# Kernel tuning notes

Hardware: AMD Instinct MI355X
Metric: run time of the kernel (lower is better)

The kernel has to match this reference:

```python
import jax, jax.numpy as jnp
import numpy as np

B, N, D, R, W, H, I = 256, 2048, 128, 4, 1, 1024, 1024
CI = I + R * D                       # controller input size (1536)
IF = 2 * D * W + 2 * W + 1 + 4 * R + D * R   # interface size (787)
OPI = H + R * D                      # output_proj input (1536)


def _norm(v):
    # F.normalize(dim=-1): x / max(||x||, eps)
    return v / jnp.maximum(jnp.linalg.norm(v, axis=-1, keepdims=True), 1e-12)


def setup_inputs() -> dict:
    key = jax.random.key(0)
    ks = jax.random.split(key, 16)
    u = lambda k, shape, fan: jax.random.uniform(k, shape, jnp.float32, -1.0 / np.sqrt(fan), 1.0 / np.sqrt(fan))
    return {
        "x": jax.random.normal(ks[0], (B, I), jnp.float32),
        "memory": jax.random.normal(ks[1], (N, D), jnp.float32) * np.sqrt(2.0 / (N + D)),  # xavier-ish
        "usage": jax.random.uniform(ks[2], (N,), jnp.float32),          # usage in [0,1)
        "link": jax.random.normal(ks[3], (N, N), jnp.float32) * 0.01,   # non-trivial link state
        "W_ih": u(ks[4], (4 * H, CI), H),
        "W_hh": u(ks[5], (4 * H, H), H),
        "b_ih": u(ks[6], (4 * H,), H),
        "b_hh": u(ks[7], (4 * H,), H),
        "W_if": u(ks[8], (IF, H), H),
        "b_if": u(ks[9], (IF,), H),
        "W_out": u(ks[10], (H, OPI), OPI),
        "b_out": u(ks[11], (H,), OPI),
    }


def reference(x, memory, usage, link, W_ih, W_hh, b_ih, b_hh, W_if, b_if, W_out, b_out):
    # initial uniform read weights (prev state at first step)
    prev_rw = jnp.full((B, R, N), 1.0 / N, x.dtype)
    read_flat = (prev_rw @ memory).reshape(B, -1)                 # (B, R*D)
    cin = jnp.concatenate([x, read_flat], axis=-1)                # (B, CI)

    # single LSTM step, h0 = c0 = 0, torch gate order i,f,g,o
    g = cin @ W_ih.T + b_ih + b_hh
    gi, gf, gg, go = jnp.split(g, 4, axis=-1)
    c = jax.nn.sigmoid(gi) * jnp.tanh(gg)
    h = jax.nn.sigmoid(go) * jnp.tanh(c)                          # (B, H) controller out

    itf = h @ W_if.T + b_if                                       # (B, IF)
    o = 0
    write_vals = itf[:, o:o + D * W].reshape(B, W, D); o += D * W
    erase = jax.nn.sigmoid(itf[:, o:o + D * W]).reshape(B, W, D); o += D * W
    write_gates = jax.nn.sigmoid(itf[:, o:o + W]); o += W         # (B, W)
    alloc_gate = jax.nn.sigmoid(itf[:, o:o + 1]); o += 1          # (B, 1)
    o += W                                                        # free gates (parsed, unused)
    read_modes = jax.nn.softmax(itf[:, o:o + 3 * R].reshape(B, R, 3), -1); o += 3 * R
    read_str = jax.nn.softplus(itf[:, o:o + R]); o += R           # (B, R)
    read_keys = itf[:, o:o + D * R].reshape(B, R, D)

    # content addressing for the write (strength = 1)
    mem_n = _norm(memory)
    cw = jax.nn.softmax(_norm(write_vals.mean(1)) @ mem_n.T, -1)  # (B, N)

    # allocation weighting: sorted-usage cumprod (per source semantics)
    idx = jnp.argsort(usage)
    su = usage[idx]
    cp = jnp.cumprod(1.0 - su)
    alloc_s = jnp.concatenate([su[:1], su[1:] * cp[:-1]])
    alloc = jnp.zeros_like(usage).at[idx].set(alloc_s)[None, :] * alloc_gate  # (B, N)

    write_w = write_gates[:, :, None] * (0.5 * cw + 0.5 * alloc)[:, None, :]  # (B, W, N)

    # temporal link update: batch-mean of diag-masked outer product, decay 0.9
    lu = jnp.einsum('bwn,bwm->nm', write_w, write_w) / B
    lu = lu * (1.0 - jnp.eye(N, dtype=lu.dtype))
    link_new = link * 0.9 + lu * 0.1

    # memory write (erase then add, batch-mean)
    ev = erase * write_gates[:, :, None]
    av = write_vals * write_gates[:, :, None]
    erase_mat = jnp.einsum('bwn,bwd->nd', write_w, ev) / B
    add_mat = jnp.einsum('bwn,bwd->nd', write_w, av) / B
    mem_new = memory * (1.0 - erase_mat) + add_mat

    # read addressing on updated memory and updated link (all R heads vectorized)
    sim = jnp.einsum('brd,nd->brn', _norm(read_keys), _norm(mem_new))
    content_r = jax.nn.softmax(sim * read_str[:, :, None], -1)    # (B, R, N)
    backward_w = jnp.einsum('brn,nm->brm', prev_rw, link_new)     # mode 1: prev @ L
    forward_w = jnp.einsum('brn,mn->brm', prev_rw, link_new)      # mode 2: prev @ L^T
    new_rw = (read_modes[..., 0:1] * content_r
              + read_modes[..., 1:2] * backward_w
              + read_modes[..., 2:3] * forward_w)                 # (B, R, N)

    read_out = (new_rw @ mem_new).reshape(B, -1)                  # (B, R*D)
    out = jnp.concatenate([h, read_out], axis=-1) @ W_out.T + b_out
    return out
```

## Files before the change

### kernel.cpp

```cpp
#include <hip/hip_runtime.h>
#include <cmath>

#define DEVI __device__ __forceinline__

DEVI float sigm(float x){ return 1.f/(1.f+expf(-x)); }

typedef __attribute__((ext_vector_type(8))) _Float16 half8;
typedef __attribute__((ext_vector_type(4))) _Float16 half4;
typedef __attribute__((ext_vector_type(4))) float float4v;


__global__ void k_zero(float* __restrict__ p, int n){
  int i = blockIdx.x*256 + threadIdx.x;
  if (i < n) p[i] = 0.f;
}

__global__ __launch_bounds__(256) void k_stage1(
    const float* __restrict__ mem, float* __restrict__ cm, _Float16* __restrict__ mem_h,
    const float* __restrict__ usage, float* __restrict__ alloc,
    const float* __restrict__ link, float* __restrict__ rsl, float* __restrict__ cslp)
{
  __shared__ float smem[4][132];
  const int blk = blockIdx.x, t = threadIdx.x;
  const int wv = t >> 6, lane = t & 63;

  if (blk < 128){
    int rbase = blk*16 + wv*4;
    float x0[4], x1[4], ss[4];
    #pragma unroll
    for (int u = 0; u < 4; u++){
      const float* a = mem + (size_t)(rbase+u)*128;
      x0[u] = a[lane]; x1[u] = a[lane+64];
    }
    #pragma unroll
    for (int u = 0; u < 4; u++) ss[u] = x0[u]*x0[u] + x1[u]*x1[u];
    #pragma unroll
    for (int o = 1; o < 64; o <<= 1){
      #pragma unroll
      for (int u = 0; u < 4; u++) ss[u] += __shfl_xor(ss[u], o);
    }
    float c0 = 0.f, c1 = 0.f;
    #pragma unroll
    for (int u = 0; u < 4; u++){
      float invn = 1.f / fmaxf(sqrtf(ss[u]), 1e-12f);
      mem_h[(size_t)(rbase+u)*128 + lane]      = (_Float16)(x0[u]*invn);
      mem_h[(size_t)(rbase+u)*128 + 64 + lane] = (_Float16)(x1[u]*invn);
      c0 += x0[u]; c1 += x1[u];
    }
    smem[wv][lane] = c0; smem[wv][64+lane] = c1;
    __syncthreads();
    if (t < 128) atomicAdd(&cm[t], smem[0][t]+smem[1][t]+smem[2][t]+smem[3][t]);
  } else if (blk < 384){
    int pb = blk - 128;
    int r0 = pb*8;
    int c0 = t*8;
    float4v v0[8], v1[8];
    #pragma unroll
    for (int u = 0; u < 8; u++){
      const float* lp = link + (size_t)(r0+u)*2048 + c0;
      v0[u] = *(const float4v*)lp;
      v1[u] = *(const float4v*)(lp+4);
    }
    float colacc[8];
    #pragma unroll
    for (int j = 0; j < 8; j++) colacc[j] = 0.f;
    float rowpart[8];
    #pragma unroll
    for (int u = 0; u < 8; u++){
      float s = 0.f;
      #pragma unroll
      for (int j = 0; j < 4; j++){
        colacc[j]   += v0[u][j]; colacc[4+j] += v1[u][j];
        s += v0[u][j] + v1[u][j];
      }
      rowpart[u] = s;
    }
    #pragma unroll
    for (int o = 1; o < 64; o <<= 1){
      #pragma unroll
      for (int u = 0; u < 8; u++) rowpart[u] += __shfl_xor(rowpart[u], o);
    }
    if (lane == 0){
      #pragma unroll
      for (int u = 0; u < 8; u++) smem[wv][u] = rowpart[u];
    }
    __syncthreads();
    if (t < 8) rsl[r0+t] = smem[0][t]+smem[1][t]+smem[2][t]+smem[3][t];
    float4v w0, w1;
    #pragma unroll
    for (int j = 0; j < 4; j++){ w0[j] = colacc[j]; w1[j] = colacc[4+j]; }
    *(float4v*)&cslp[(size_t)pb*2048 + c0]     = w0;
    *(float4v*)&cslp[(size_t)pb*2048 + c0 + 4] = w1;
  } else {
    int n = (blk - 384)*4 + wv;
    float un = usage[n];
    float prod = 1.f;
    #pragma unroll
    for (int i = 0; i < 32; i++){
      int m = lane + i*64;
      float um = usage[m];
      bool before = (um < un) || (um == un && m < n);
      prod *= before ? (1.f - um) : 1.f;
    }
    #pragma unroll
    for (int o = 32; o > 0; o >>= 1) prod *= __shfl_xor(prod, o);
    if (lane == 0) alloc[n] = un * prod;
  }
}

#define QA 264
#define QB 520
#define QB3 776

template<typename TB> struct BReg;
template<> struct BReg<_Float16>{
  half8 v;
  DEVI void load(const _Float16* p){ v = *(const half8*)p; }
  DEVI half8 get() const { return v; }
};
template<> struct BReg<float>{
  float4v a, b;
  DEVI void load(const float* p){ a = *(const float4v*)p; b = *(const float4v*)(p+4); }
  DEVI half8 get() const {
    half8 h;
    #pragma unroll
    for (int j = 0; j < 4; j++){ h[j] = (_Float16)a[j]; h[4+j] = (_Float16)b[j]; }
    return h;
  }
};

struct ARegX {
  float4v a, b; float sc;
  DEVI void load(const float* __restrict__ x, const float* __restrict__ cm, int row, int k){
    const float* p;
    if (k < 1024){ p = x + (size_t)row*1024 + k; sc = 1.f; }
    else         { p = cm + ((k - 1024) & 127); sc = (1.f/2048.f); }
    a = *(const float4v*)p; b = *(const float4v*)(p+4);
  }
  DEVI half8 get() const {
    half8 h;
    #pragma unroll
    for (int j = 0; j < 4; j++){ h[j] = (_Float16)(a[j]*sc); h[4+j] = (_Float16)(b[j]*sc); }
    return h;
  }
};

template<typename TB>
__global__ __launch_bounds__(256) void gemm_t(
    const _Float16* __restrict__ A, const TB* __restrict__ Bm, float* __restrict__ C,
    int M, int N, int K,
    const float* __restrict__ bias1, const float* __restrict__ bias2)
{
  __shared__ _Float16 Ah[2][8*QA];
  __shared__ _Float16 Bh[2][8*QB];
  const int tid = threadIdx.x;
  const int m0 = blockIdx.y*32, n0 = blockIdx.x*64;
  const int T = K >> 6;
  const int arow = tid >> 3, aq = tid & 7;
  const int brow = tid >> 3, bq = tid & 7;
  int nB0 = n0 + brow;      if (nB0 >= N) nB0 = N - 1;
  int nB1 = n0 + brow + 32; if (nB1 >= N) nB1 = N - 1;
  const _Float16* Aptr = A + (size_t)(m0 + arow)*K + aq*8;
  const TB* Bp0 = Bm + (size_t)nB0*K + bq*8;
  const TB* Bp1 = Bm + (size_t)nB1*K + bq*8;
  const int wA  = aq*QA + arow*8;
  const int wB0 = bq*QB + brow*8;
  const int wB1 = bq*QB + (brow+32)*8;
  const int wv_ = tid >> 6, lane = tid & 63;
  const int fq = lane >> 4, fr = lane & 15;
  const int m16 = (wv_ & 1)*16, nb = (wv_ >> 1)*32;

  half8 ra;
  BReg<TB> rb0, rb1;
  ra = *(const half8*)(Aptr);
  rb0.load(Bp0);
  rb1.load(Bp1);
  *(half8*)&Ah[0][wA]  = ra;
  *(half8*)&Bh[0][wB0] = rb0.get();
  *(half8*)&Bh[0][wB1] = rb1.get();
  __syncthreads();

  float4v acc0 = {0.f,0.f,0.f,0.f}, acc1 = {0.f,0.f,0.f,0.f};
  for (int t = 0; t < T; t++){
    const int cur = t & 1, nxt = cur ^ 1;
    if (t+1 < T){
      ra = *(const half8*)(Aptr + (t+1)*64);
      rb0.load(Bp0 + (t+1)*64);
      rb1.load(Bp1 + (t+1)*64);
    }
    #pragma unroll
    for (int s = 0; s < 2; s++){
      int q = s*4 + fq;
      half8 a  = *(half8*)&Ah[cur][q*QA + (m16+fr)*8];
      half8 b0 = *(half8*)&Bh[cur][q*QB + (nb+fr)*8];
      half8 b1 = *(half8*)&Bh[cur][q*QB + (nb+16+fr)*8];
      acc0 = __builtin_amdgcn_mfma_f32_16x16x32_f16(a, b0, acc0, 0, 0, 0);
      acc1 = __builtin_amdgcn_mfma_f32_16x16x32_f16(a, b1, acc1, 0, 0, 0);
    }
    if (t+1 < T){
      *(half8*)&Ah[nxt][wA]  = ra;
      *(half8*)&Bh[nxt][wB0] = rb0.get();
      *(half8*)&Bh[nxt][wB1] = rb1.get();
    }
    __syncthreads();
  }

  const int colA = n0 + nb + fr, colB = colA + 16;
  #pragma unroll
  for (int i = 0; i < 4; i++){
    int m = m0 + m16 + fq*4 + i;
    if (colA < N){
      float v = acc0[i];
      if (bias1) v += bias1[colA];
      if (bias2) v += bias2[colA];
      C[(size_t)m*N + colA] = v;
    }
    if (colB < N){
      float v = acc1[i];
      if (bias1) v += bias1[colB];
      if (bias2) v += bias2[colB];
      C[(size_t)m*N + colB] = v;
    }
  }
}

__global__ __launch_bounds__(256) void k_gemm_wwExp(
    const _Float16* __restrict__ A, const _Float16* __restrict__ Bm,
    float* __restrict__ C, float* __restrict__ rsum)
{
  __shared__ _Float16 Ah[2][8*QA];
  __shared__ _Float16 Bh[2][8*QB];
  const int tid = threadIdx.x;
  const int m0 = blockIdx.y*32, n0 = blockIdx.x*64;
  const int arow = tid >> 3, aq = tid & 7;
  const int brow = tid >> 3, bq = tid & 7;
  const _Float16* Aptr = A + (size_t)(m0 + arow)*128 + aq*8;
  const _Float16* Bp0 = Bm + (size_t)(n0 + brow)*128 + bq*8;
  const _Float16* Bp1 = Bm + (size_t)(n0 + brow + 32)*128 + bq*8;
  const int wA  = aq*QA + arow*8;
  const int wB0 = bq*QB + brow*8;
  const int wB1 = bq*QB + (brow+32)*8;
  const int wv_ = tid >> 6, lane = tid & 63;
  const int fq = lane >> 4, fr = lane & 15;
  const int m16 = (wv_ & 1)*16, nb = (wv_ >> 1)*32;

  half8 ra  = *(const half8*)(Aptr);
  half8 rb0 = *(const half8*)(Bp0);
  half8 rb1 = *(const half8*)(Bp1);
  *(half8*)&Ah[0][wA]  = ra;
  *(half8*)&Bh[0][wB0] = rb0;
  *(half8*)&Bh[0][wB1] = rb1;
  __syncthreads();

  float4v acc0 = {0.f,0.f,0.f,0.f}, acc1 = {0.f,0.f,0.f,0.f};
  for (int t = 0; t < 2; t++){
    const int cur = t & 1, nxt = cur ^ 1;
    if (t == 0){
      ra  = *(const half8*)(Aptr + 64);
      rb0 = *(const half8*)(Bp0 + 64);
      rb1 = *(const half8*)(Bp1 + 64);
    }
    #pragma unroll
    for (int s = 0; s < 2; s++){
      int q = s*4 + fq;
      half8 a  = *(half8*)&Ah[cur][q*QA + (m16+fr)*8];
      half8 b0 = *(half8*)&Bh[cur][q*QB + (nb+fr)*8];
      half8 b1 = *(half8*)&Bh[cur][q*QB + (nb+16+fr)*8];
      acc0 = __builtin_amdgcn_mfma_f32_16x16x32_f16(a, b0, acc0, 0, 0, 0);
      acc1 = __builtin_amdgcn_mfma_f32_16x16x32_f16(a, b1, acc1, 0, 0, 0);
    }
    if (t == 0){
      *(half8*)&Ah[nxt][wA]  = ra;
      *(half8*)&Bh[nxt][wB0] = rb0;
      *(half8*)&Bh[nxt][wB1] = rb1;
    }
    __syncthreads();
  }

  const int colA = n0 + nb + fr, colB = colA + 16;
  #pragma unroll
  for (int i = 0; i < 4; i++){
    int m = m0 + m16 + fq*4 + i;
    float e0 = expf(acc0[i]);
    float e1 = expf(acc1[i]);
    C[(size_t)m*2048 + colA] = e0;
    C[(size_t)m*2048 + colB] = e1;
    float rs = e0 + e1;
    #pragma unroll
    for (int o = 1; o < 16; o <<= 1) rs += __shfl_xor(rs, o);
    if (fr == 0) atomicAdd(&rsum[m], rs);
  }
}

__global__ __launch_bounds__(256) void k_gemm_lstm(
    const float* __restrict__ x, const float* __restrict__ cm,
    const float* __restrict__ W,
    const float* __restrict__ b_ih, const float* __restrict__ b_hh,
    _Float16* __restrict__ h)
{
  __shared__ _Float16 Ah[2][8*QA];
  __shared__ _Float16 Bh[2][8*QB3];
  const int tid = threadIdx.x;
  const int m0 = blockIdx.y*32, c0 = blockIdx.x*32;
  const int T = 24;
  const int arow = tid >> 3, aq = tid & 7;
  const int brow = tid >> 3, bq = tid & 7;
  const int arw = m0 + arow;
  const float* Bpi = W + (size_t)(       c0 + brow)*1536 + bq*8;
  const float* Bpg = W + (size_t)(2048 + c0 + brow)*1536 + bq*8;
  const float* Bpo = W + (size_t)(3072 + c0 + brow)*1536 + bq*8;
  const int wA  = aq*QA + arow*8;
  const int wBi = bq*QB3 + brow*8;
  const int wBg = bq*QB3 + (32+brow)*8;
  const int wBo = bq*QB3 + (64+brow)*8;
  const int wv_ = tid >> 6, lane = tid & 63;
  const int fq = lane >> 4, fr = lane & 15;
  const int m16 = (wv_ & 1)*16, c16 = (wv_ >> 1)*16;

  ARegX ax0, ax1;
  BReg<float> ri0, rg0, ro0, ri1, rg1, ro1;
  ax0.load(x, cm, arw, aq*8);
  ri0.load(Bpi); rg0.load(Bpg); ro0.load(Bpo);
  ax1.load(x, cm, arw, aq*8 + 64);
  ri1.load(Bpi + 64); rg1.load(Bpg + 64); ro1.load(Bpo + 64);
  *(half8*)&Ah[0][wA]  = ax0.get();
  *(half8*)&Bh[0][wBi] = ri0.get();
  *(half8*)&Bh[0][wBg] = rg0.get();
  *(half8*)&Bh[0][wBo] = ro0.get();
  __syncthreads();

  float4v acci = {0.f,0.f,0.f,0.f}, accg = {0.f,0.f,0.f,0.f}, acco = {0.f,0.f,0.f,0.f};
  for (int t = 0; t < T; t++){
    const int cur = t & 1, nxt = cur ^ 1;
    if (t+2 < T){
      if (cur == 0){
        ax0.load(x, cm, arw, aq*8 + (t+2)*64);
        ri0.load(Bpi + (t+2)*64); rg0.load(Bpg + (t+2)*64); ro0.load(Bpo + (t+2)*64);
      } else {
        ax1.load(x, cm, arw, aq*8 + (t+2)*64);
        ri1.load(Bpi + (t+2)*64); rg1.load(Bpg + (t+2)*64); ro1.load(Bpo + (t+2)*64);
      }
    }
    #pragma unroll
    for (int s = 0; s < 2; s++){
      int q = s*4 + fq;
      half8 a  = *(half8*)&Ah[cur][q*QA + (m16+fr)*8];
      half8 bi = *(half8*)&Bh[cur][q*QB3 + (c16+fr)*8];
      half8 bg = *(half8*)&Bh[cur][q*QB3 + (32+c16+fr)*8];
      half8 bo = *(half8*)&Bh[cur][q*QB3 + (64+c16+fr)*8];
      acci = __builtin_amdgcn_mfma_f32_16x16x32_f16(a, bi, acci, 0, 0, 0);
      accg = __builtin_amdgcn_mfma_f32_16x16x32_f16(a, bg, accg, 0, 0, 0);
      acco = __builtin_amdgcn_mfma_f32_16x16x32_f16(a, bo, acco, 0, 0, 0);
    }
    if (t+1 < T){
      if (nxt == 1){
        *(half8*)&Ah[1][wA]  = ax1.get();
        *(half8*)&Bh[1][wBi] = ri1.get();
        *(half8*)&Bh[1][wBg] = rg1.get();
        *(half8*)&Bh[1][wBo] = ro1.get();
      } else {
        *(half8*)&Ah[0][wA]  = ax0.get();
        *(half8*)&Bh[0][wBi] = ri0.get();
        *(half8*)&Bh[0][wBg] = rg0.get();
        *(half8*)&Bh[0][wBo] = ro0.get();
      }
    }
    __syncthreads();
  }

  const int col = c0 + c16 + fr;
  const float bi1 = b_ih[col]        + b_hh[col];
  const float bg1 = b_ih[2048 + col] + b_hh[2048 + col];
  const float bo1 = b_ih[3072 + col] + b_hh[3072 + col];
  #pragma unroll
  for (int i = 0; i < 4; i++){
    int m = m0 + m16 + fq*4 + i;
    float gi = acci[i] + bi1;
    float gg = accg[i] + bg1;
    float go = acco[i] + bo1;
    float c = sigm(gi) * tanhf(gg);
    h[(size_t)m*1024 + col] = (_Float16)(sigm(go) * tanhf(c));
  }
}

DEVI float blockReduce128(float v, float* lds2){
  #pragma unroll
  for (int o = 32; o > 0; o >>= 1) v += __shfl_xor(v, o);
  int w = threadIdx.x >> 6;
  __syncthreads();
  if ((threadIdx.x & 63) == 0) lds2[w] = v;
  __syncthreads();
  return lds2[0] + lds2[1];
}

__global__ __launch_bounds__(128) void k_parse(const float* __restrict__ itf,
    _Float16* __restrict__ wv_h, float* __restrict__ ev, float* __restrict__ av,
    float* __restrict__ wg_, float* __restrict__ ag_,
    float* __restrict__ rm0, float* __restrict__ rm1, float* __restrict__ rm2,
    _Float16* __restrict__ rks_h)
{
  __shared__ float red[2];
  int b = blockIdx.x, t = threadIdx.x;
  const float* it = itf + (size_t)b*787;
  float wg = sigm(it[256]);
  float ag = sigm(it[257]);
  if (t == 0){ wg_[b] = wg; ag_[b] = ag; }
  float w = it[t];
  av[b*128 + t] = w * wg;
  ev[b*128 + t] = sigm(it[128 + t]) * wg;
  float ss = blockReduce128(w*w, red);
  float invwv = 1.f / fmaxf(sqrtf(ss), 1e-12f);
  wv_h[b*128 + t] = (_Float16)(w * invwv);
  if (t < 4){
    int rr = t;
    float m0v = it[259 + rr*3 + 0], m1v = it[259 + rr*3 + 1], m2v = it[259 + rr*3 + 2];
    float mx = fmaxf(m0v, fmaxf(m1v, m2v));
    float e0 = expf(m0v - mx), e1 = expf(m1v - mx), e2 = expf(m2v - mx);
    float inv = 1.f / (e0 + e1 + e2);
    rm0[b*4 + rr] = e0*inv; rm1[b*4 + rr] = e1*inv; rm2[b*4 + rr] = e2*inv;
  }
  #pragma unroll
  for (int rr = 0; rr < 4; rr++){
    float kv = it[275 + rr*128 + t];
    float ks = blockReduce128(kv*kv, red);
    float sx = it[271 + rr];
    float str = fmaxf(sx, 0.f) + log1pf(expf(-fabsf(sx)));
    float invk = 1.f / fmaxf(sqrtf(ks), 1e-12f);
    rks_h[((size_t)b*4 + rr)*128 + t] = (_Float16)(kv * invk * str);
  }
}

__global__ __launch_bounds__(256) void k_memupdate_fused(const float* __restrict__ ww,
    const float* __restrict__ ev, const float* __restrict__ av,
    const float* __restrict__ mem,
    const float* __restrict__ wg, const float* __restrict__ ag,
    const float* __restrict__ alloc, const float* __restrict__ rsum,
    const float* __restrict__ rsl, const float* __restrict__ cslp,
    _Float16* __restrict__ memn_h, _Float16* __restrict__ memnT_h,
    float* __restrict__ bwm, float* __restrict__ fwm)
{
  __shared__ float Ws[16][34];
  __shared__ float Es[16][132], Vs[16][132];
  __shared__ float lb[128], lf[128];
  __shared__ _Float16 Traw[32][132];
  __shared__ float tbs[256], c1s[256], c2s[256];
  __shared__ float allocL[32];
  __shared__ float sq[8][32], sd[8][32];
  __shared__ float cpart[8][32];
  __shared__ float bwL[32], fwL[32];
  __shared__ float sred[4];
  const int n0 = blockIdx.x*32;
  const int tid = threadIdx.x, tx = tid & 31, ty = tid >> 5;

  {
    float sa = 0.f;
    #pragma unroll
    for (int i = 0; i < 8; i++) sa += alloc[tid + i*256];
    #pragma unroll
    for (int o = 32; o > 0; o >>= 1) sa += __shfl_xor(sa, o);
    if ((tid & 63) == 0) sred[tid >> 6] = sa;
    if (tid < 128){ lb[tid] = 0.f; lf[tid] = 0.f; }
    if (tid < 32) allocL[tid] = alloc[n0 + tid];
    __syncthreads();
    sa = (sred[0]+sred[1]) + (sred[2]+sred[3]);
    float w = wg[tid], a = ag[tid];
    tbs[tid] = w*(0.5f + 0.5f*a*sa);
    c1s[tid] = 0.5f*w / rsum[tid];
    c2s[tid] = 0.5f*w*a;
  }
  {
    int col = n0 + tx;
    float s = 0.f;
    for (int p = ty*32; p < ty*32 + 32; p += 4){
      s += cslp[(size_t)(p+0)*2048 + col] + cslp[(size_t)(p+1)*2048 + col]
         + cslp[(size_t)(p+2)*2048 + col] + cslp[(size_t)(p+3)*2048 + col];
    }
    cpart[ty][tx] = s;
  }
  __syncthreads();

  const int wk = tid >> 4, wn = (tid & 15)*2;
  const int ek = tid >> 4, ec = (tid & 15)*8;
  float ae[4][4] = {}, aa[4][4] = {};
  float qp = 0.f, ddp = 0.f;
  for (int k0 = 0; k0 < 256; k0 += 16){
    float2 vw  = *(const float2*)(ww + (size_t)(k0+wk)*2048 + n0 + wn);
    float4 ve0 = *(const float4*)(ev + (size_t)(k0+ek)*128 + ec);
    float4 ve1 = *(const float4*)(ev + (size_t)(k0+ek)*128 + ec + 4);
    float4 va0 = *(const float4*)(av + (size_t)(k0+ek)*128 + ec);
    float4 va1 = *(const float4*)(av + (size_t)(k0+ek)*128 + ec + 4);
    __syncthreads();
    {
      float cb1 = c1s[k0+wk], cb2 = c2s[k0+wk];
      Ws[wk][wn]   = cb1*vw.x + cb2*allocL[wn];
      Ws[wk][wn+1] = cb1*vw.y + cb2*allocL[wn+1];
    }
    *(float4*)&Es[ek][ec] = ve0; *(float4*)&Es[ek][ec+4] = ve1;
    *(float4*)&Vs[ek][ec] = va0; *(float4*)&Vs[ek][ec+4] = va1;
    __syncthreads();
    #pragma unroll
    for (int k = 0; k < 16; k++){
      float a[4], e[4], v[4];
      #pragma unroll
      for (int i = 0; i < 4; i++) a[i] = Ws[k][ty*4+i];
      #pragma unroll
      for (int j = 0; j < 4; j++){ e[j] = Es[k][tx*4+j]; v[j] = Vs[k][tx*4+j]; }
      #pragma unroll
      for (int i = 0; i < 4; i++)
        #pragma unroll
        for (int j = 0; j < 4; j++){
          ae[i][j] = fmaf(a[i], e[j], ae[i][j]);
          aa[i][j] = fmaf(a[i], v[j], aa[i][j]);
        }
    }
    {
      float w0 = Ws[ty*2+0][tx], w1 = Ws[ty*2+1][tx];
      qp  = fmaf(tbs[k0+ty*2+0], w0, qp);  ddp = fmaf(w0, w0, ddp);
      qp  = fmaf(tbs[k0+ty*2+1], w1, qp);  ddp = fmaf(w1, w1, ddp);
    }
  }
  sq[ty][tx] = qp; sd[ty][tx] = ddp;
  __syncthreads();
  if (tid < 32){
    float q = 0.f, dd = 0.f, cs = 0.f;
    #pragma unroll
    for (int z = 0; z < 8; z++){ q += sq[z][tid]; dd += sd[z][tid]; cs += cpart[z][tid]; }
    float lus = (q - dd) * (1.f/256.f);
    bwL[tid] = (0.9f*cs + 0.1f*lus) * (1.f/2048.f);
    fwL[tid] = (0.9f*rsl[n0+tid] + 0.1f*lus) * (1.f/2048.f);
  }
  __syncthreads();

  float ab[4] = {0,0,0,0}, af[4] = {0,0,0,0};
  #pragma unroll
  for (int i = 0; i < 4; i++){
    int n = n0 + ty*4 + i;
    float bwn = bwL[ty*4+i], fwn = fwL[ty*4+i];
    float v[4]; float ss = 0.f;
    #pragma unroll
    for (int j = 0; j < 4; j++){
      int d = tx*4 + j;
      float em = ae[i][j]*(1.f/256.f), am = aa[i][j]*(1.f/256.f);
      float mv = mem[(size_t)n*128 + d]*(1.f - em) + am;
      v[j] = mv; ss += mv*mv;
      ab[j] = fmaf(bwn, mv, ab[j]);
      af[j] = fmaf(fwn, mv, af[j]);
    }
    #pragma unroll
    for (int o = 1; o < 32; o <<= 1) ss += __shfl_xor(ss, o);
    float invn = 1.f / fmaxf(sqrtf(ss), 1e-12f);
    half4 hn, hr;
    #pragma unroll
    for (int j = 0; j < 4; j++){ hn[j] = (_Float16)(v[j]*invn); hr[j] = (_Float16)v[j]; }
    *(half4*)(memn_h + (size_t)n*128 + tx*4) = hn;
    *(half4*)&Traw[ty*4+i][tx*4] = hr;
  }
  __syncthreads();
  {
    int d = tid >> 1, seg = (tid & 1)*16;
    half8 o0, o1;
    #pragma unroll
    for (int j = 0; j < 8; j++){ o0[j] = Traw[seg+j][d]; o1[j] = Traw[seg+8+j][d]; }
    *(half8*)(memnT_h + (size_t)d*2048 + n0 + seg)     = o0;
    *(half8*)(memnT_h + (size_t)d*2048 + n0 + seg + 8) = o1;
  }
  #pragma unroll
  for (int j = 0; j < 4; j++){
    atomicAdd(&lb[tx*4+j], ab[j]);
    atomicAdd(&lf[tx*4+j], af[j]);
  }
  __syncthreads();
  if (tid < 128){
    atomicAdd(&bwm[tid], lb[tid]);
    atomicAdd(&fwm[tid], lf[tid]);
  }
}

__global__ __launch_bounds__(256) void k_flash(
    const _Float16* __restrict__ Q, const _Float16* __restrict__ Kh,
    const _Float16* __restrict__ Vt,
    float* __restrict__ pacc, float* __restrict__ pm, float* __restrict__ pl)
{
  __shared__ _Float16 Pl[4][16][32];
  __shared__ float cmb[4][2080];
  __shared__ float scl[4][16];
  const int tid = threadIdx.x;
  const int qt = blockIdx.x >> 2, kc = blockIdx.x & 3;
  const int wv = tid >> 6, lane = tid & 63;
  const int fq = lane >> 4, fr = lane & 15;
  const int kw0 = kc*512 + wv*128;

  half8 aq[4];
  #pragma unroll
  for (int c = 0; c < 4; c++)
    aq[c] = *(const half8*)(Q + (size_t)(qt*16 + fr)*128 + c*32 + fq*8);

  float m[4] = {-3.0e38f,-3.0e38f,-3.0e38f,-3.0e38f};
  float l[4] = {0.f,0.f,0.f,0.f};
  float4v acc[8] = {};
  for (int s = 0; s < 4; s++){
    const int kb = kw0 + s*32;
    float4v S0 = {0,0,0,0}, S1 = {0,0,0,0};
    #pragma unroll
    for (int c = 0; c < 4; c++){
      half8 b0 = *(const half8*)(Kh + (size_t)(kb + fr)*128      + c*32 + fq*8);
      half8 b1 = *(const half8*)(Kh + (size_t)(kb + 16 + fr)*128 + c*32 + fq*8);
      S0 = __builtin_amdgcn_mfma_f32_16x16x32_f16(aq[c], b0, S0, 0, 0, 0);
      S1 = __builtin_amdgcn_mfma_f32_16x16x32_f16(aq[c], b1, S1, 0, 0, 0);
    }
    float mt[4], ps[4];
    #pragma unroll
    for (int i = 0; i < 4; i++) mt[i] = fmaxf(S0[i], S1[i]);
    #pragma unroll
    for (int o = 1; o < 16; o <<= 1){
      #pragma unroll
      for (int i = 0; i < 4; i++) mt[i] = fmaxf(mt[i], __shfl_xor(mt[i], o));
    }
    #pragma unroll
    for (int i = 0; i < 4; i++){
      float mn = fmaxf(m[i], mt[i]);
      float al = expf(m[i] - mn);
      float p0 = expf(S0[i] - mn), p1 = expf(S1[i] - mn);
      S0[i] = p0; S1[i] = p1;
      ps[i] = p0 + p1;
      l[i] *= al;
      m[i] = mn;
      #pragma unroll
      for (int c = 0; c < 8; c++) acc[c][i] *= al;
    }
    #pragma unroll
    for (int o = 1; o < 16; o <<= 1){
      #pragma unroll
      for (int i = 0; i < 4; i++) ps[i] += __shfl_xor(ps[i], o);
    }
    #pragma unroll
    for (int i = 0; i < 4; i++) l[i] += ps[i];
    #pragma unroll
    for (int i = 0; i < 4; i++){
      Pl[wv][fq*4+i][fr]      = (_Float16)S0[i];
      Pl[wv][fq*4+i][16 + fr] = (_Float16)S1[i];
    }
    half8 pf = *(half8*)&Pl[wv][fr][fq*8];
    #pragma unroll
    for (int c = 0; c < 8; c++){
      half8 bv = *(const half8*)(Vt + (size_t)(c*16 + fr)*2048 + kb + fq*8);
      acc[c] = __builtin_amdgcn_mfma_f32_16x16x32_f16(pf, bv, acc[c], 0, 0, 0);
    }
  }
  if (fr == 0){
    #pragma unroll
    for (int i = 0; i < 4; i++){
      cmb[wv][fq*4+i]      = m[i];
      cmb[wv][16 + fq*4+i] = l[i];
    }
  }
  #pragma unroll
  for (int c = 0; c < 8; c++)
    #pragma unroll
    for (int i = 0; i < 4; i++)
      cmb[wv][32 + (fq*4+i)*128 + c*16 + fr] = acc[c][i];
  __syncthreads();
  if (tid < 16){
    float mm = fmaxf(fmaxf(cmb[0][tid], cmb[1][tid]), fmaxf(cmb[2][tid], cmb[3][tid]));
    float ll = 0.f;
    #pragma unroll
    for (int w = 0; w < 4; w++){
      float e = expf(cmb[w][tid] - mm);
      scl[w][tid] = e;
      ll += e * cmb[w][16 + tid];
    }
    pm[blockIdx.x*16 + tid] = mm;
    pl[blockIdx.x*16 + tid] = ll;
  }
  __syncthreads();
  for (int e = tid; e < 2048; e += 256){
    int q = e >> 7;
    float a = scl[0][q]*cmb[0][32+e] + scl[1][q]*cmb[1][32+e]
            + scl[2][q]*cmb[2][32+e] + scl[3][q]*cmb[3][32+e];
    pacc[(size_t)blockIdx.x*2048 + e] = a;
  }
}

__global__ void k_hro_comb(const _Float16* __restrict__ h, const float* __restrict__ pacc,
                           const float* __restrict__ pm, const float* __restrict__ pl,
                           const float* __restrict__ rm0, const float* __restrict__ rm1,
                           const float* __restrict__ rm2, const float* __restrict__ bwm,
                           const float* __restrict__ fwm, _Float16* __restrict__ hro){
  int idx = blockIdx.x*256 + threadIdx.x;
  int b = idx / 1536, k = idx - b*1536;
  if (k < 1024){
    hro[idx] = h[b*1024 + k];
  } else {
    int r = k - 1024, rh = r >> 7, d = r & 127;
    int row = b*4 + rh, qt = row >> 4, q = row & 15;
    float mm = -3.0e38f;
    #pragma unroll
    for (int kc = 0; kc < 4; kc++) mm = fmaxf(mm, pm[(qt*4+kc)*16 + q]);
    float num = 0.f, den = 0.f;
    #pragma unroll
    for (int kc = 0; kc < 4; kc++){
      float e = expf(pm[(qt*4+kc)*16 + q] - mm);
      den += e * pl[(qt*4+kc)*16 + q];
      num += e * pacc[(size_t)(qt*4+kc)*2048 + q*128 + d];
    }
    float pv = num / den;
    hro[idx] = (_Float16)(rm0[row]*pv + rm1[row]*bwm[d] + rm2[row]*fwm[d]);
  }
}


extern "C" void kernel_launch(void* const* d_in, const int* in_sizes, int n_in,
                              void* d_out, int out_size, void* d_ws, size_t ws_size,
                              hipStream_t stream)
{
  const float* x     = (const float*)d_in[0];
  const float* mem   = (const float*)d_in[1];
  const float* usage = (const float*)d_in[2];
  const float* link  = (const float*)d_in[3];
  const float* W_ih  = (const float*)d_in[4];
  const float* b_ih  = (const float*)d_in[6];
  const float* b_hh  = (const float*)d_in[7];
  const float* W_if  = (const float*)d_in[8];
  const float* b_if  = (const float*)d_in[9];
  const float* W_out = (const float*)d_in[10];
  const float* b_out = (const float*)d_in[11];
  float* out = (float*)d_out;
  float* ws  = (float*)d_ws;

  float* cm     = ws + 0;
  float* bwm    = ws + 2176;
  float* fwm    = ws + 2304;
  float* rsum   = ws + 2432;
  float* wg     = ws + 6784;
  float* ag     = ws + 7040;
  float* rm0    = ws + 7296;
  float* rm1    = ws + 8320;
  float* rm2    = ws + 9344;
  float* alloc  = ws + 10368;
  float* rsl    = ws + 12416;
  float* ev     = ws + 14464;
  float* av     = ws + 47232;
  float* itf    = ws + 1128576;
  float* ww     = ws + 1330048;
  float* pacc   = ws + 1854336;
  float* pm     = ws + 2378624;
  float* pl     = ws + 2382720;
  _Float16* wv_h    = (_Float16*)(ws + 2386816);
  _Float16* mem_h   = (_Float16*)(ws + 2403200);
  _Float16* memn_h  = (_Float16*)(ws + 2534272);
  _Float16* memnT_h = (_Float16*)(ws + 2665344);
  _Float16* rks_h   = (_Float16*)(ws + 2796416);
  _Float16* hro_h   = (_Float16*)(ws + 2861952);
  _Float16* h_h     = (_Float16*)(ws + 3255168);
  float* cslp       = ws + 3386240;

  k_zero<<<11, 256, 0, stream>>>(ws, 2688);

  k_stage1<<<896, 256, 0, stream>>>(mem, cm, mem_h, usage, alloc, link, rsl, cslp);

  k_gemm_lstm<<<dim3(32,8), 256, 0, stream>>>(x, cm, W_ih, b_ih, b_hh, h_h);

  gemm_t<float><<<dim3(13,8), 256, 0, stream>>>(h_h, W_if, itf, 256, 787, 1024, b_if, nullptr);
  k_parse<<<256, 128, 0, stream>>>(itf, wv_h, ev, av, wg, ag, rm0, rm1, rm2, rks_h);

  k_gemm_wwExp<<<dim3(32,8), 256, 0, stream>>>(wv_h, mem_h, ww, rsum);

  k_memupdate_fused<<<64, 256, 0, stream>>>(ww, ev, av, mem, wg, ag, alloc, rsum,
                                            rsl, cslp, memn_h, memnT_h, bwm, fwm);

  k_flash<<<256, 256, 0, stream>>>(rks_h, memn_h, memnT_h, pacc, pm, pl);

  k_hro_comb<<<1536, 256, 0, stream>>>(h_h, pacc, pm, pl, rm0, rm1, rm2, bwm, fwm, hro_h);
  gemm_t<float><<<dim3(16,8), 256, 0, stream>>>(hro_h, W_out, out, 256, 1024, 1536, b_out, nullptr);

  (void)in_sizes; (void)n_in; (void)out_size; (void)ws_size;
}
```

Before: 233.8 us.

## Co-schedule link/alloc reductions with LSTM GEMM and drop h copy before output GEMM

```diff
diff --git a/kernel.cpp b/kernel.cpp
--- a/kernel.cpp
+++ b/kernel.cpp
@@ -16,96 +16,36 @@
 }
 
 __global__ __launch_bounds__(256) void k_stage1(
-    const float* __restrict__ mem, float* __restrict__ cm, _Float16* __restrict__ mem_h,
-    const float* __restrict__ usage, float* __restrict__ alloc,
-    const float* __restrict__ link, float* __restrict__ rsl, float* __restrict__ cslp)
+    const float* __restrict__ mem, float* __restrict__ cm, _Float16* __restrict__ mem_h)
 {
   __shared__ float smem[4][132];
   const int blk = blockIdx.x, t = threadIdx.x;
   const int wv = t >> 6, lane = t & 63;
-
-  if (blk < 128){
-    int rbase = blk*16 + wv*4;
-    float x0[4], x1[4], ss[4];
-    #pragma unroll
-    for (int u = 0; u < 4; u++){
-      const float* a = mem + (size_t)(rbase+u)*128;
-      x0[u] = a[lane]; x1[u] = a[lane+64];
-    }
-    #pragma unroll
-    for (int u = 0; u < 4; u++) ss[u] = x0[u]*x0[u] + x1[u]*x1[u];
-    #pragma unroll
-    for (int o = 1; o < 64; o <<= 1){
-      #pragma unroll
-      for (int u = 0; u < 4; u++) ss[u] += __shfl_xor(ss[u], o);
-    }
-    float c0 = 0.f, c1 = 0.f;
-    #pragma unroll
-    for (int u = 0; u < 4; u++){
-      float invn = 1.f / fmaxf(sqrtf(ss[u]), 1e-12f);
-      mem_h[(size_t)(rbase+u)*128 + lane]      = (_Float16)(x0[u]*invn);
-      mem_h[(size_t)(rbase+u)*128 + 64 + lane] = (_Float16)(x1[u]*invn);
-      c0 += x0[u]; c1 += x1[u];
-    }
-    smem[wv][lane] = c0; smem[wv][64+lane] = c1;
-    __syncthreads();
-    if (t < 128) atomicAdd(&cm[t], smem[0][t]+smem[1][t]+smem[2][t]+smem[3][t]);
-  } else if (blk < 384){
-    int pb = blk - 128;
-    int r0 = pb*8;
-    int c0 = t*8;
-    float4v v0[8], v1[8];
-    #pragma unroll
-    for (int u = 0; u < 8; u++){
-      const float* lp = link + (size_t)(r0+u)*2048 + c0;
-      v0[u] = *(const float4v*)lp;
-      v1[u] = *(const float4v*)(lp+4);
-    }
-    float colacc[8];
-    #pragma unroll
-    for (int j = 0; j < 8; j++) colacc[j] = 0.f;
-    float rowpart[8];
-    #pragma unroll
-    for (int u = 0; u < 8; u++){
-      float s = 0.f;
-      #pragma unroll
-      for (int j = 0; j < 4; j++){
-        colacc[j]   += v0[u][j]; colacc[4+j] += v1[u][j];
-        s += v0[u][j] + v1[u][j];
-      }
-      rowpart[u] = s;
-    }
-    #pragma unroll
-    for (int o = 1; o < 64; o <<= 1){
-      #pragma unroll
-      for (int u = 0; u < 8; u++) rowpart[u] += __shfl_xor(rowpart[u], o);
-    }
-    if (lane == 0){
-      #pragma unroll
-      for (int u = 0; u < 8; u++) smem[wv][u] = rowpart[u];
-    }
-    __syncthreads();
-    if (t < 8) rsl[r0+t] = smem[0][t]+smem[1][t]+smem[2][t]+smem[3][t];
-    float4v w0, w1;
-    #pragma unroll
-    for (int j = 0; j < 4; j++){ w0[j] = colacc[j]; w1[j] = colacc[4+j]; }
-    *(float4v*)&cslp[(size_t)pb*2048 + c0]     = w0;
-    *(float4v*)&cslp[(size_t)pb*2048 + c0 + 4] = w1;
-  } else {
-    int n = (blk - 384)*4 + wv;
-    float un = usage[n];
-    float prod = 1.f;
-    #pragma unroll
-    for (int i = 0; i < 32; i++){
-      int m = lane + i*64;
-      float um = usage[m];
-      bool before = (um < un) || (um == un && m < n);
-      prod *= before ? (1.f - um) : 1.f;
-    }
-    #pragma unroll
-    for (int o = 32; o > 0; o >>= 1) prod *= __shfl_xor(prod, o);
-    if (lane == 0) alloc[n] = un * prod;
-  }
+  int rbase = blk*16 + wv*4;
+  float x0[4], x1[4], ss[4];
+  #pragma unroll
+  for (int u = 0; u < 4; u++){
+    const float* a = mem + (size_t)(rbase+u)*128;
+    x0[u] = a[lane]; x1[u] = a[lane+64];
+  }
+  #pragma unroll
+  for (int u = 0; u < 4; u++) ss[u] = x0[u]*x0[u] + x1[u]*x1[u];
+  #pragma unroll
+  for (int o = 1; o < 64; o <<= 1){
+    #pragma unroll
+    for (int u = 0; u < 4; u++) ss[u] += __shfl_xor(ss[u], o);
+  }
+  float c0 = 0.f, c1 = 0.f;
+  #pragma unroll
+  for (int u = 0; u < 4; u++){
+    float invn = 1.f / fmaxf(sqrtf(ss[u]), 1e-12f);
+    mem_h[(size_t)(rbase+u)*128 + lane]      = (_Float16)(x0[u]*invn);
+    mem_h[(size_t)(rbase+u)*128 + 64 + lane] = (_Float16)(x1[u]*invn);
+    c0 += x0[u]; c1 += x1[u];
+  }
+  smem[wv][lane] = c0; smem[wv][64+lane] = c1;
+  __syncthreads();
+  if (t < 128) atomicAdd(&cm[t], smem[0][t]+smem[1][t]+smem[2][t]+smem[3][t]);
 }
 
 #define QA 264
@@ -224,6 +164,78 @@
   }
 }
 
+__global__ __launch_bounds__(256) void gemm_hro(
+    const _Float16* __restrict__ Ah_, const _Float16* __restrict__ Aro,
+    const float* __restrict__ Bm, float* __restrict__ C,
+    const float* __restrict__ bias1)
+{
+  __shared__ _Float16 Ah[2][8*QA];
+  __shared__ _Float16 Bh[2][8*QB];
+  const int tid = threadIdx.x;
+  const int m0 = blockIdx.y*32, n0 = blockIdx.x*64;
+  const int T = 24;
+  const int arow = tid >> 3, aq = tid & 7;
+  const int brow = tid >> 3, bq = tid & 7;
+  const int arw = m0 + arow;
+  const float* Bp0 = Bm + (size_t)(n0 + brow)*1536 + bq*8;
+  const float* Bp1 = Bm + (size_t)(n0 + brow + 32)*1536 + bq*8;
+  const int wA  = aq*QA + arow*8;
+  const int wB0 = bq*QB + brow*8;
+  const int wB1 = bq*QB + (brow+32)*8;
+  const int wv_ = tid >> 6, lane = tid & 63;
+  const int fq = lane >> 4, fr = lane & 15;
+  const int m16 = (wv_ & 1)*16, nb = (wv_ >> 1)*32;
+
+  auto ldA = [&](int k) -> half8 {
+    const _Float16* p = (k < 1024) ? (Ah_ + (size_t)arw*1024 + k)
+                                   : (Aro + (size_t)arw*512 + (k - 1024));
+    return *(const half8*)p;
+  };
+
+  half8 ra;
+  BReg<float> rb0, rb1;
+  ra = ldA(aq*8);
+  rb0.load(Bp0);
+  rb1.load(Bp1);
+  *(half8*)&Ah[0][wA]  = ra;
+  *(half8*)&Bh[0][wB0] = rb0.get();
+  *(half8*)&Bh[0][wB1] = rb1.get();
+  __syncthreads();
+
+  float4v acc0 = {0.f,0.f,0.f,0.f}, acc1 = {0.f,0.f,0.f,0.f};
+  for (int t = 0; t < T; t++){
+    const int cur = t & 1, nxt = cur ^ 1;
+    if (t+1 < T){
+      ra = ldA(aq*8 + (t+1)*64);
+      rb0.load(Bp0 + (t+1)*64);
+      rb1.load(Bp1 + (t+1)*64);
+    }
+    #pragma unroll
+    for (int s = 0; s < 2; s++){
+      int q = s*4 + fq;
+      half8 a  = *(half8*)&Ah[cur][q*QA + (m16+fr)*8];
+      half8 b0 = *(half8*)&Bh[cur][q*QB + (nb+fr)*8];
+      half8 b1 = *(half8*)&Bh[cur][q*QB + (nb+16+fr)*8];
+      acc0 = __builtin_amdgcn_mfma_f32_16x16x32_f16(a, b0, acc0, 0, 0, 0);
+      acc1 = __builtin_amdgcn_mfma_f32_16x16x32_f16(a, b1, acc1, 0, 0, 0);
+    }
+    if (t+1 < T){
+      *(half8*)&Ah[nxt][wA]  = ra;
+      *(half8*)&Bh[nxt][wB0] = rb0.get();
+      *(half8*)&Bh[nxt][wB1] = rb1.get();
+    }
+    __syncthreads();
+  }
+
+  const int colA = n0 + nb + fr, colB = colA + 16;
+  #pragma unroll
+  for (int i = 0; i < 4; i++){
+    int m = m0 + m16 + fq*4 + i;
+    C[(size_t)m*1024 + colA] = acc0[i] + bias1[colA];
+    C[(size_t)m*1024 + colB] = acc1[i] + bias1[colB];
+  }
+}
+
 __global__ __launch_bounds__(256) void k_gemm_wwExp(
     const _Float16* __restrict__ A, const _Float16* __restrict__ Bm,
     float* __restrict__ C, float* __restrict__ rsum)
@@ -292,94 +304,157 @@
   }
 }
 
-__global__ __launch_bounds__(256) void k_gemm_lstm(
+__global__ __launch_bounds__(256) void k_big2(
     const float* __restrict__ x, const float* __restrict__ cm,
     const float* __restrict__ W,
     const float* __restrict__ b_ih, const float* __restrict__ b_hh,
-    _Float16* __restrict__ h)
+    _Float16* __restrict__ h,
+    const float* __restrict__ usage, float* __restrict__ alloc,
+    const float* __restrict__ link, float* __restrict__ rsl, float* __restrict__ cslp)
 {
-  __shared__ _Float16 Ah[2][8*QA];
-  __shared__ _Float16 Bh[2][8*QB3];
-  const int tid = threadIdx.x;
-  const int m0 = blockIdx.y*32, c0 = blockIdx.x*32;
-  const int T = 24;
-  const int arow = tid >> 3, aq = tid & 7;
-  const int brow = tid >> 3, bq = tid & 7;
-  const int arw = m0 + arow;
-  const float* Bpi = W + (size_t)(       c0 + brow)*1536 + bq*8;
-  const float* Bpg = W + (size_t)(2048 + c0 + brow)*1536 + bq*8;
-  const float* Bpo = W + (size_t)(3072 + c0 + brow)*1536 + bq*8;
-  const int wA  = aq*QA + arow*8;
-  const int wBi = bq*QB3 + brow*8;
-  const int wBg = bq*QB3 + (32+brow)*8;
-  const int wBo = bq*QB3 + (64+brow)*8;
-  const int wv_ = tid >> 6, lane = tid & 63;
-  const int fq = lane >> 4, fr = lane & 15;
-  const int m16 = (wv_ & 1)*16, c16 = (wv_ >> 1)*16;
-
-  ARegX ax0, ax1;
-  BReg<float> ri0, rg0, ro0, ri1, rg1, ro1;
-  ax0.load(x, cm, arw, aq*8);
-  ri0.load(Bpi); rg0.load(Bpg); ro0.load(Bpo);
-  ax1.load(x, cm, arw, aq*8 + 64);
-  ri1.load(Bpi + 64); rg1.load(Bpg + 64); ro1.load(Bpo + 64);
-  *(half8*)&Ah[0][wA]  = ax0.get();
-  *(half8*)&Bh[0][wBi] = ri0.get();
-  *(half8*)&Bh[0][wBg] = rg0.get();
-  *(half8*)&Bh[0][wBo] = ro0.get();
-  __syncthreads();
-
-  float4v acci = {0.f,0.f,0.f,0.f}, accg = {0.f,0.f,0.f,0.f}, acco = {0.f,0.f,0.f,0.f};
-  for (int t = 0; t < T; t++){
-    const int cur = t & 1, nxt = cur ^ 1;
-    if (t+2 < T){
-      if (cur == 0){
-        ax0.load(x, cm, arw, aq*8 + (t+2)*64);
-        ri0.load(Bpi + (t+2)*64); rg0.load(Bpg + (t+2)*64); ro0.load(Bpo + (t+2)*64);
-      } else {
-        ax1.load(x, cm, arw, aq*8 + (t+2)*64);
-        ri1.load(Bpi + (t+2)*64); rg1.load(Bpg + (t+2)*64); ro1.load(Bpo + (t+2)*64);
+  extern __shared__ char smraw[];
+  const int blk = blockIdx.x, tid = threadIdx.x;
+  const int wv = tid >> 6, lane = tid & 63;
+
+  if (blk < 256){
+    _Float16* AhP = (_Float16*)smraw;
+    _Float16* BhP = (_Float16*)(smraw + 2*8*QA*sizeof(_Float16));
+    const int SA = 8*QA, SB = 8*QB3;
+    const int m0 = (blk >> 5)*32, c0 = (blk & 31)*32;
+    const int T = 24;
+    const int arow = tid >> 3, aq = tid & 7;
+    const int brow = tid >> 3, bq = tid & 7;
+    const int arw = m0 + arow;
+    const float* Bpi = W + (size_t)(       c0 + brow)*1536 + bq*8;
+    const float* Bpg = W + (size_t)(2048 + c0 + brow)*1536 + bq*8;
+    const float* Bpo = W + (size_t)(3072 + c0 + brow)*1536 + bq*8;
+    const int wA  = aq*QA + arow*8;
+    const int wBi = bq*QB3 + brow*8;
+    const int wBg = bq*QB3 + (32+brow)*8;
+    const int wBo = bq*QB3 + (64+brow)*8;
+    const int fq = lane >> 4, fr = lane & 15;
+    const int m16 = (wv & 1)*16, c16 = (wv >> 1)*16;
+
+    ARegX ax0, ax1;
+    BReg<float> ri0, rg0, ro0, ri1, rg1, ro1;
+    ax0.load(x, cm, arw, aq*8);
+    ri0.load(Bpi); rg0.load(Bpg); ro0.load(Bpo);
+    ax1.load(x, cm, arw, aq*8 + 64);
+    ri1.load(Bpi + 64); rg1.load(Bpg + 64); ro1.load(Bpo + 64);
+    *(half8*)&AhP[wA]  = ax0.get();
+    *(half8*)&BhP[wBi] = ri0.get();
+    *(half8*)&BhP[wBg] = rg0.get();
+    *(half8*)&BhP[wBo] = ro0.get();
+    __syncthreads();
+
+    float4v acci = {0.f,0.f,0.f,0.f}, accg = {0.f,0.f,0.f,0.f}, acco = {0.f,0.f,0.f,0.f};
+    for (int t = 0; t < T; t++){
+      const int cur = t & 1, nxt = cur ^ 1;
+      if (t+2 < T){
+        if (cur == 0){
+          ax0.load(x, cm, arw, aq*8 + (t+2)*64);
+          ri0.load(Bpi + (t+2)*64); rg0.load(Bpg + (t+2)*64); ro0.load(Bpo + (t+2)*64);
+        } else {
+          ax1.load(x, cm, arw, aq*8 + (t+2)*64);
+          ri1.load(Bpi + (t+2)*64); rg1.load(Bpg + (t+2)*64); ro1.load(Bpo + (t+2)*64);
+        }
       }
-    }
-    #pragma unroll
-    for (int s = 0; s < 2; s++){
-      int q = s*4 + fq;
-      half8 a  = *(half8*)&Ah[cur][q*QA + (m16+fr)*8];
-      half8 bi = *(half8*)&Bh[cur][q*QB3 + (c16+fr)*8];
-      half8 bg = *(half8*)&Bh[cur][q*QB3 + (32+c16+fr)*8];
-      half8 bo = *(half8*)&Bh[cur][q*QB3 + (64+c16+fr)*8];
-      acci = __builtin_amdgcn_mfma_f32_16x16x32_f16(a, bi, acci, 0, 0, 0);
-      accg = __builtin_amdgcn_mfma_f32_16x16x32_f16(a, bg, accg, 0, 0, 0);
-      acco = __builtin_amdgcn_mfma_f32_16x16x32_f16(a, bo, acco, 0, 0, 0);
-    }
-    if (t+1 < T){
-      if (nxt == 1){
-        *(half8*)&Ah[1][wA]  = ax1.get();
-        *(half8*)&Bh[1][wBi] = ri1.get();
-        *(half8*)&Bh[1][wBg] = rg1.get();
-        *(half8*)&Bh[1][wBo] = ro1.get();
-      } else {
-        *(half8*)&Ah[0][wA]  = ax0.get();
-        *(half8*)&Bh[0][wBi] = ri0.get();
-        *(half8*)&Bh[0][wBg] = rg0.get();
-        *(half8*)&Bh[0][wBo] = ro0.get();
+      #pragma unroll
+      for (int s = 0; s < 2; s++){
+        int q = s*4 + fq;
+        half8 a  = *(half8*)&AhP[cur*SA + q*QA + (m16+fr)*8];
+        half8 bi = *(half8*)&BhP[cur*SB + q*QB3 + (c16+fr)*8];
+        half8 bg = *(half8*)&BhP[cur*SB + q*QB3 + (32+c16+fr)*8];
+        half8 bo = *(half8*)&BhP[cur*SB + q*QB3 + (64+c16+fr)*8];
+        acci = __builtin_amdgcn_mfma_f32_16x16x32_f16(a, bi, acci, 0, 0, 0);
+        accg = __builtin_amdgcn_mfma_f32_16x16x32_f16(a, bg, accg, 0, 0, 0);
+        acco = __builtin_amdgcn_mfma_f32_16x16x32_f16(a, bo, acco, 0, 0, 0);
       }
+      if (t+1 < T){
+        if (nxt == 1){
+          *(half8*)&AhP[SA + wA]  = ax1.get();
+          *(half8*)&BhP[SB + wBi] = ri1.get();
+          *(half8*)&BhP[SB + wBg] = rg1.get();
+          *(half8*)&BhP[SB + wBo] = ro1.get();
+        } else {
+          *(half8*)&AhP[wA]  = ax0.get();
+          *(half8*)&BhP[wBi] = ri0.get();
+          *(half8*)&BhP[wBg] = rg0.get();
+          *(half8*)&BhP[wBo] = ro0.get();
+        }
+      }
+      __syncthreads();
+    }
+
+    const int col = c0 + c16 + fr;
+    const float bi1 = b_ih[col]        + b_hh[col];
+    const float bg1 = b_ih[2048 + col] + b_hh[2048 + col];
+    const float bo1 = b_ih[3072 + col] + b_hh[3072 + col];
+    #pragma unroll
+    for (int i = 0; i < 4; i++){
+      int m = m0 + m16 + fq*4 + i;
+      float gi = acci[i] + bi1;
+      float gg = accg[i] + bg1;
+      float go = acco[i] + bo1;
+      float c = sigm(gi) * tanhf(gg);
+      h[(size_t)m*1024 + col] = (_Float16)(sigm(go) * tanhf(c));
+    }
+  } else if (blk < 512){
+    float (*smem)[132] = (float(*)[132])smraw;
+    int pb = blk - 256;
+    int r0 = pb*8;
+    int c0 = tid*8;
+    float4v v0[8], v1[8];
+    #pragma unroll
+    for (int u = 0; u < 8; u++){
+      const float* lp = link + (size_t)(r0+u)*2048 + c0;
+      v0[u] = *(const float4v*)lp;
+      v1[u] = *(const float4v*)(lp+4);
+    }
+    float colacc[8];
+    #pragma unroll
+    for (int j = 0; j < 8; j++) colacc[j] = 0.f;
+    float rowpart[8];
+    #pragma unroll
+    for (int u = 0; u < 8; u++){
+      float s = 0.f;
+      #pragma unroll
+      for (int j = 0; j < 4; j++){
+        colacc[j]   += v0[u][j]; colacc[4+j] += v1[u][j];
+        s += v0[u][j] + v1[u][j];
+      }
+      rowpart[u] = s;
+    }
+    #pragma unroll
+    for (int o = 1; o < 64; o <<= 1){
+      #pragma unroll
+      for (int u = 0; u < 8; u++) rowpart[u] += __shfl_xor(rowpart[u], o);
+    }
+    if (lane == 0){
+      #pragma unroll
+      for (int u = 0; u < 8; u++) smem[wv][u] = rowpart[u];
     }
     __syncthreads();
-  }
-
-  const int col = c0 + c16 + fr;
-  const float bi1 = b_ih[col]        + b_hh[col];
-  const float bg1 = b_ih[2048 + col] + b_hh[2048 + col];
-  const float bo1 = b_ih[3072 + col] + b_hh[3072 + col];
-  #pragma unroll
-  for (int i = 0; i < 4; i++){
-    int m = m0 + m16 + fq*4 + i;
-    float gi = acci[i] + bi1;
-    float gg = accg[i] + bg1;
-    float go = acco[i] + bo1;
-    float c = sigm(gi) * tanhf(gg);
-    h[(size_t)m*1024 + col] = (_Float16)(sigm(go) * tanhf(c));
+    if (tid < 8) rsl[r0+tid] = smem[0][tid]+smem[1][tid]+smem[2][tid]+smem[3][tid];
+    float4v w0, w1;
+    #pragma unroll
+    for (int j = 0; j < 4; j++){ w0[j] = colacc[j]; w1[j] = colacc[4+j]; }
+    *(float4v*)&cslp[(size_t)pb*2048 + c0]     = w0;
+    *(float4v*)&cslp[(size_t)pb*2048 + c0 + 4] = w1;
+  } else {
+    int n = (blk - 512)*4 + wv;
+    float un = usage[n];
+    float prod = 1.f;
+    #pragma unroll
+    for (int i = 0; i < 32; i++){
+      int m = lane + i*64;
+      float um = usage[m];
+      bool before = (um < un) || (um == un && m < n);
+      prod *= before ? (1.f - um) : 1.f;
+    }
+    #pragma unroll
+    for (int o = 32; o > 0; o >>= 1) prod *= __shfl_xor(prod, o);
+    if (lane == 0) alloc[n] = un * prod;
   }
 }
 
@@ -681,31 +756,26 @@
   }
 }
 
-__global__ void k_hro_comb(const _Float16* __restrict__ h, const float* __restrict__ pacc,
-                           const float* __restrict__ pm, const float* __restrict__ pl,
-                           const float* __restrict__ rm0, const float* __restrict__ rm1,
-                           const float* __restrict__ rm2, const float* __restrict__ bwm,
-                           const float* __restrict__ fwm, _Float16* __restrict__ hro){
+__global__ void k_ro(const float* __restrict__ pacc, const float* __restrict__ pm,
+                     const float* __restrict__ pl,
+                     const float* __restrict__ rm0, const float* __restrict__ rm1,
+                     const float* __restrict__ rm2, const float* __restrict__ bwm,
+                     const float* __restrict__ fwm, _Float16* __restrict__ ro){
   int idx = blockIdx.x*256 + threadIdx.x;
-  int b = idx / 1536, k = idx - b*1536;
-  if (k < 1024){
-    hro[idx] = h[b*1024 + k];
-  } else {
-    int r = k - 1024, rh = r >> 7, d = r & 127;
-    int row = b*4 + rh, qt = row >> 4, q = row & 15;
-    float mm = -3.0e38f;
-    #pragma unroll
-    for (int kc = 0; kc < 4; kc++) mm = fmaxf(mm, pm[(qt*4+kc)*16 + q]);
-    float num = 0.f, den = 0.f;
-    #pragma unroll
-    for (int kc = 0; kc < 4; kc++){
-      float e = expf(pm[(qt*4+kc)*16 + q] - mm);
-      den += e * pl[(qt*4+kc)*16 + q];
-      num += e * pacc[(size_t)(qt*4+kc)*2048 + q*128 + d];
-    }
-    float pv = num / den;
-    hro[idx] = (_Float16)(rm0[row]*pv + rm1[row]*bwm[d] + rm2[row]*fwm[d]);
-  }
+  int row = idx >> 7, d = idx & 127;
+  int qt = row >> 4, q = row & 15;
+  float mm = -3.0e38f;
+  #pragma unroll
+  for (int kc = 0; kc < 4; kc++) mm = fmaxf(mm, pm[(qt*4+kc)*16 + q]);
+  float num = 0.f, den = 0.f;
+  #pragma unroll
+  for (int kc = 0; kc < 4; kc++){
+    float e = expf(pm[(qt*4+kc)*16 + q] - mm);
+    den += e * pl[(qt*4+kc)*16 + q];
+    num += e * pacc[(size_t)(qt*4+kc)*2048 + q*128 + d];
+  }
+  float pv = num / den;
+  ro[idx] = (_Float16)(rm0[row]*pv + rm1[row]*bwm[d] + rm2[row]*fwm[d]);
 }
 
 
@@ -750,15 +820,18 @@
   _Float16* memn_h  = (_Float16*)(ws + 2534272);
   _Float16* memnT_h = (_Float16*)(ws + 2665344);
   _Float16* rks_h   = (_Float16*)(ws + 2796416);
-  _Float16* hro_h   = (_Float16*)(ws + 2861952);
+  _Float16* ro_h    = (_Float16*)(ws + 2861952);
   _Float16* h_h     = (_Float16*)(ws + 3255168);
   float* cslp       = ws + 3386240;
 
+  const int SH_BIG2 = (2*8*QA + 2*8*QB3) * (int)sizeof(_Float16);
+
   k_zero<<<11, 256, 0, stream>>>(ws, 2688);
 
-  k_stage1<<<896, 256, 0, stream>>>(mem, cm, mem_h, usage, alloc, link, rsl, cslp);
-
-  k_gemm_lstm<<<dim3(32,8), 256, 0, stream>>>(x, cm, W_ih, b_ih, b_hh, h_h);
+  k_stage1<<<128, 256, 0, stream>>>(mem, cm, mem_h);
+
+  k_big2<<<1024, 256, SH_BIG2, stream>>>(x, cm, W_ih, b_ih, b_hh, h_h,
+                                         usage, alloc, link, rsl, cslp);
 
   gemm_t<float><<<dim3(13,8), 256, 0, stream>>>(h_h, W_if, itf, 256, 787, 1024, b_if, nullptr);
   k_parse<<<256, 128, 0, stream>>>(itf, wv_h, ev, av, wg, ag, rm0, rm1, rm2, rks_h);
@@ -770,8 +843,8 @@
 
   k_flash<<<256, 256, 0, stream>>>(rks_h, memn_h, memnT_h, pacc, pm, pl);
 
-  k_hro_comb<<<1536, 256, 0, stream>>>(h_h, pacc, pm, pl, rm0, rm1, rm2, bwm, fwm, hro_h);
-  gemm_t<float><<<dim3(16,8), 256, 0, stream>>>(hro_h, W_out, out, 256, 1024, 1536, b_out, nullptr);
+  k_ro<<<512, 256, 0, stream>>>(pacc, pm, pl, rm0, rm1, rm2, bwm, fwm, ro_h);
+  gemm_hro<<<dim3(16,8), 256, 0, stream>>>(h_h, ro_h, W_out, out, b_out);
 
   (void)in_sizes; (void)n_in; (void)out_size; (void)ws_size;
 }
```

New measurement: 230.2 us. No clear change (-1.6%).
